# Kernel optimization log

Measured on AMD Instinct MI355X. Metric: run time of the kernel, lower is better.

The kernel has to match this reference:

```python
import jax, jax.numpy as jnp
import numpy as np

N = 30000
E = 600000
IN = 64
HID = 128
EPS = 1e-5
HEADS_PER_LAYER = (4, 4, 1)


def _bn(x, g, b):
    # eval-mode BatchNorm: running_mean=0, running_var=1
    return x * (g / np.sqrt(1.0 + EPS)) + b


def _segment_softmax(e, dst, n):
    m = jax.ops.segment_max(e, dst, num_segments=n)
    ex = jnp.exp(e - m[dst])
    s = jax.ops.segment_sum(ex, dst, num_segments=n)
    return ex / (s[dst] + 1e-16)


def _gcn_conv(x, w, b, src, dst, norm, n):
    m = (x @ w)[src] * norm[:, None]            # [E+N, HID]
    return jax.ops.segment_sum(m, dst, num_segments=n) + b


def _gat_conv(x, w, a_src, a_dst, b, src, dst, n, heads):
    C = HID // heads
    xh = (x @ w).reshape(n, heads, C)
    asrc = (xh * a_src.reshape(heads, C)).sum(-1)   # [N, heads]
    adst = (xh * a_dst.reshape(heads, C)).sum(-1)
    e = jax.nn.leaky_relu(asrc[src] + adst[dst], 0.2)  # [E+N, heads]
    alpha = _segment_softmax(e, dst, n)
    out = jax.ops.segment_sum(xh[src] * alpha[:, :, None], dst, num_segments=n)
    return out.reshape(n, HID) + b


def _forward(x, gcn_in_w, gcn_in_b, gcn_res_w, gcn_res_b, gcn_w, gcn_b,
             gcn_bn_g, gcn_bn_b, gcn_c1w, gcn_c1b, gcn_c2w, gcn_c2b,
             gcn_c3w, gcn_c3b, gat_in_w, gat_in_b, gat_w, gat_asrc,
             gat_adst, gat_b, gat_bn_g, gat_bn_b, feat_imp, gat_c1w,
             gat_c1b, gat_cbn_g, gat_cbn_b, gat_c2w, gat_c2b, gat_c3w,
             gat_c3b, fin_w, fin_b, fin_bn_g, fin_bn_b, fin2_w, fin2_b,
             edge_index):
    n = x.shape[0]
    loop = jnp.arange(n, dtype=edge_index.dtype)
    src = jnp.concatenate([edge_index[0], loop])  # add self-loops
    dst = jnp.concatenate([edge_index[1], loop])
    # GCN symmetric normalization (with self-loops)
    deg = jax.ops.segment_sum(jnp.ones_like(dst, dtype=x.dtype), dst, num_segments=n)
    dis = jnp.where(deg > 0, jax.lax.rsqrt(jnp.maximum(deg, 1.0)), 0.0)
    norm = dis[src] * dis[dst]

    # ---- GCN branch (eval: dropout = identity, self-attn skipped since N>5000) ----
    xp = x @ gcn_in_w + gcn_in_b
    res = x @ gcn_res_w + gcn_res_b
    for i in range(3):
        xn = _gcn_conv(xp, gcn_w[i], gcn_b[i], src, dst, norm, n)
        xn = jax.nn.relu(_bn(xn, gcn_bn_g[i], gcn_bn_b[i]))
        if i % 2 == 1:
            xp = xn + res
            res = xp
        else:
            xp = xn
    h = jax.nn.relu(xp @ gcn_c1w + gcn_c1b)
    h = jax.nn.relu(h @ gcn_c2w + gcn_c2b)
    gcn_out = h @ gcn_c3w + gcn_c3b

    # ---- GAT branch ----
    xg = x @ gat_in_w + gat_in_b
    for i in range(3):
        xg = _gat_conv(xg, gat_w[i], gat_asrc[i], gat_adst[i], gat_b[i],
                       src, dst, n, HEADS_PER_LAYER[i])
        xg = jax.nn.elu(_bn(xg, gat_bn_g[i], gat_bn_b[i]))
    xg = xg * feat_imp
    h = jax.nn.relu(xg @ gat_c1w + gat_c1b)
    h = _bn(h, gat_cbn_g, gat_cbn_b)
    h = jax.nn.relu(h @ gat_c2w + gat_c2b)
    gat_out = h @ gat_c3w + gat_c3b

    # ---- fusion: N > 10000 -> weighted blend path ----
    fused = 0.6 * gcn_out + 0.4 * gat_out
    h = jax.nn.relu(fused @ fin_w + fin_b)
    h = _bn(h, fin_bn_g, fin_bn_b)
    return h @ fin2_w + fin2_b  # [N, 2]


def setup_inputs() -> dict:
    key = jax.random.key(0)
    ks = iter(jax.random.split(key, 64))

    def nrm(shape, scale=1.0):
        return jax.random.normal(next(ks), shape, dtype=jnp.float32) * scale

    s_in = 1.0 / np.sqrt(IN)
    s_h = 1.0 / np.sqrt(HID)
    inp = {}
    inp['x'] = nrm((N, IN))
    inp['edge_index'] = jax.random.randint(next(ks), (2, E), 0, N, dtype=jnp.int32)
    inp['gcn_in_w'] = nrm((IN, HID), s_in); inp['gcn_in_b'] = nrm((HID,), 0.01)
    inp['gcn_res_w'] = nrm((IN, HID), s_in); inp['gcn_res_b'] = nrm((HID,), 0.01)
    inp['gcn_w'] = nrm((3, HID, HID), s_h); inp['gcn_b'] = nrm((3, HID), 0.01)
    inp['gcn_bn_g'] = 1.0 + nrm((3, HID), 0.1); inp['gcn_bn_b'] = nrm((3, HID), 0.1)
    inp['gcn_c1w'] = nrm((HID, 64), s_h); inp['gcn_c1b'] = nrm((64,), 0.01)
    inp['gcn_c2w'] = nrm((64, 32), 0.125); inp['gcn_c2b'] = nrm((32,), 0.01)
    inp['gcn_c3w'] = nrm((32, HID), 0.18); inp['gcn_c3b'] = nrm((HID,), 0.01)
    inp['gat_in_w'] = nrm((IN, HID), s_in); inp['gat_in_b'] = nrm((HID,), 0.01)
    inp['gat_w'] = nrm((3, HID, HID), s_h)
    inp['gat_asrc'] = nrm((3, HID), s_h); inp['gat_adst'] = nrm((3, HID), s_h)
    inp['gat_b'] = nrm((3, HID), 0.01)
    inp['gat_bn_g'] = 1.0 + nrm((3, HID), 0.1); inp['gat_bn_b'] = nrm((3, HID), 0.1)
    inp['feat_imp'] = 1.0 + nrm((HID,), 0.1)
    inp['gat_c1w'] = nrm((HID, 64), s_h); inp['gat_c1b'] = nrm((64,), 0.01)
    inp['gat_cbn_g'] = 1.0 + nrm((64,), 0.1); inp['gat_cbn_b'] = nrm((64,), 0.1)
    inp['gat_c2w'] = nrm((64, 32), 0.125); inp['gat_c2b'] = nrm((32,), 0.01)
    inp['gat_c3w'] = nrm((32, HID), 0.18); inp['gat_c3b'] = nrm((HID,), 0.01)
    inp['fin_w'] = nrm((HID, 64), s_h); inp['fin_b'] = nrm((64,), 0.01)
    inp['fin_bn_g'] = 1.0 + nrm((64,), 0.1); inp['fin_bn_b'] = nrm((64,), 0.1)
    inp['fin2_w'] = nrm((64, 2), 0.125); inp['fin2_b'] = nrm((2,), 0.01)
    return inp


def reference(x, edge_index, gcn_in_w, gcn_in_b, gcn_res_w, gcn_res_b, gcn_w,
              gcn_b, gcn_bn_g, gcn_bn_b, gcn_c1w, gcn_c1b, gcn_c2w, gcn_c2b,
              gcn_c3w, gcn_c3b, gat_in_w, gat_in_b, gat_w, gat_asrc, gat_adst,
              gat_b, gat_bn_g, gat_bn_b, feat_imp, gat_c1w, gat_c1b, gat_cbn_g,
              gat_cbn_b, gat_c2w, gat_c2b, gat_c3w, gat_c3b, fin_w, fin_b,
              fin_bn_g, fin_bn_b, fin2_w, fin2_b):
    return _forward(x, gcn_in_w, gcn_in_b, gcn_res_w, gcn_res_b, gcn_w, gcn_b,
                    gcn_bn_g, gcn_bn_b, gcn_c1w, gcn_c1b, gcn_c2w, gcn_c2b,
                    gcn_c3w, gcn_c3b, gat_in_w, gat_in_b, gat_w, gat_asrc,
                    gat_adst, gat_b, gat_bn_g, gat_bn_b, feat_imp, gat_c1w,
                    gat_c1b, gat_cbn_g, gat_cbn_b, gat_c2w, gat_c2b, gat_c3w,
                    gat_c3b, fin_w, fin_b, fin_bn_g, fin_bn_b, fin2_w, fin2_b,
                    edge_index)
```

## Files before the change

kernel.cpp:

```cpp
#include <hip/hip_runtime.h>
#include <hip/hip_fp16.h>

#define RSQ_BN 0.9999950000374997f

typedef _Float16 f16x8 __attribute__((ext_vector_type(8)));
typedef float f32x4 __attribute__((ext_vector_type(4)));

union H8u { uint4 u4; __half h[8]; };
union H4u { uint2 u2; __half h[4]; };

__device__ __forceinline__ float leaky02(float x) { return x > 0.f ? x : 0.2f * x; }

__device__ __forceinline__ float4 ld4(const float* p) {
    return *reinterpret_cast<const float4*>(p);
}
__device__ __forceinline__ void ld8(float* d, const float* p) {
    float4 u = ld4(p), v = ld4(p + 4);
    d[0] = u.x; d[1] = u.y; d[2] = u.z; d[3] = u.w;
    d[4] = v.x; d[5] = v.y; d[6] = v.z; d[7] = v.w;
}


__global__ void hist_k(const int* __restrict__ edst, int* __restrict__ cnt, int E, int EN) {
    int i = blockIdx.x * 256 + threadIdx.x;
    if (i >= EN) return;
    int d = (i < E) ? edst[i] : (i - E);
    atomicAdd(&cnt[d], 1);
}

__global__ __launch_bounds__(256)
void scanA_k(const int* __restrict__ cnt, int* __restrict__ rowptr,
             int* __restrict__ bsum, int n) {
    __shared__ int sh[256];
    int t = threadIdx.x;
    int i = blockIdx.x * 256 + t;
    int v = (i < n) ? cnt[i] : 0;
    sh[t] = v;
    __syncthreads();
#pragma unroll
    for (int off = 1; off < 256; off <<= 1) {
        int u = 0;
        if (t >= off) u = sh[t - off];
        __syncthreads();
        sh[t] += u;
        __syncthreads();
    }
    if (i < n) rowptr[i] = sh[t] - v;
    if (t == 255) bsum[blockIdx.x] = sh[255];
}

__global__ __launch_bounds__(256)
void scanB_k(int* __restrict__ bsum, int nb) {
    __shared__ int sh[256];
    int t = threadIdx.x;
    int v = (t < nb) ? bsum[t] : 0;
    sh[t] = v;
    __syncthreads();
#pragma unroll
    for (int off = 1; off < 256; off <<= 1) {
        int u = 0;
        if (t >= off) u = sh[t - off];
        __syncthreads();
        sh[t] += u;
        __syncthreads();
    }
    if (t < nb) bsum[t] = sh[t] - v;
}

__global__ __launch_bounds__(256)
void scanC_k(const int* __restrict__ cnt, const int* __restrict__ bsum,
             int* __restrict__ rowptr, int* __restrict__ cursor,
             float* __restrict__ dis, int n, int EN) {
    int i = blockIdx.x * 256 + threadIdx.x;
    if (i < n) {
        int r = rowptr[i] + bsum[blockIdx.x];
        rowptr[i] = r;
        cursor[i] = r;
        dis[i] = rsqrtf((float)cnt[i]);
    }
    if (i == 0) rowptr[n] = EN;
}

__global__ void scatter_k(const int* __restrict__ esrc, const int* __restrict__ edst,
                          int* __restrict__ cursor, int* __restrict__ colidx, int E, int EN) {
    int i = blockIdx.x * 256 + threadIdx.x;
    if (i >= EN) return;
    int s, d;
    if (i < E) { s = esrc[i]; d = edst[i]; }
    else       { s = i - E; d = s; }
    int pos = atomicAdd(&cursor[d], 1);
    colidx[pos] = s;
}


__global__ void wtx_all_k(const float* __restrict__ gcn_in_w, const float* __restrict__ gcn_res_w,
                          const float* __restrict__ gat_in_w,
                          const float* __restrict__ gcn_w, const float* __restrict__ gat_w,
                          const float* __restrict__ gcn_c1w, const float* __restrict__ gat_c1w,
                          const float* __restrict__ gcn_c3w, const float* __restrict__ gat_c3w,
                          const float* __restrict__ fin_w,
                          const float* __restrict__ gcn_c2w, const float* __restrict__ gat_c2w,
                          const float* __restrict__ gat_asrc, const float* __restrict__ gat_adst,
                          __half* __restrict__ WTin, __half* __restrict__ WTg,
                          __half* __restrict__ WTa, __half* __restrict__ WTc1,
                          __half* __restrict__ WTc3, __half* __restrict__ WTfin,
                          __half* __restrict__ WTc2, __half* __restrict__ WTd) {
    int idx = blockIdx.x * 256 + threadIdx.x;
    const float* src;
    __half* dst;
    int K, M, o;
    if (idx < 24576) {
        int mi = idx >> 13; o = idx & 8191;
        src = mi == 0 ? gcn_in_w : (mi == 1 ? gcn_res_w : gat_in_w);
        dst = WTin + mi * 8192; K = 64; M = 128;
    } else if (idx < 73728) {
        int r = idx - 24576; int mi = r >> 14; o = r & 16383;
        src = gcn_w + mi * 16384; dst = WTg + mi * 16384; K = 128; M = 128;
    } else if (idx < 122880) {
        int r = idx - 73728; int mi = r >> 14; o = r & 16383;
        src = gat_w + mi * 16384; dst = WTa + mi * 16384; K = 128; M = 128;
    } else if (idx < 139264) {
        int r = idx - 122880; int mi = r >> 13; o = r & 8191;
        src = mi ? gat_c1w : gcn_c1w; dst = WTc1 + mi * 8192; K = 128; M = 64;
    } else if (idx < 147456) {
        int r = idx - 139264; int mi = r >> 12; o = r & 4095;
        src = mi ? gat_c3w : gcn_c3w; dst = WTc3 + mi * 4096; K = 32; M = 128;
    } else if (idx < 155648) {
        o = idx - 147456; src = fin_w; dst = WTfin; K = 128; M = 64;
    } else if (idx < 159744) {
        int r = idx - 155648; int mi = r >> 11; o = r & 2047;
        src = mi ? gat_c2w : gcn_c2w; dst = WTc2 + mi * 2048; K = 64; M = 32;
    } else if (idx < 165888) {
        int r = idx - 159744;
        int layer = r >> 11; o = r & 2047;
        int col = o >> 7, k = o & 127;
        int hh = (layer < 2) ? 4 : 1;
        int C = 128 / hh;
        float v = 0.f;
        if (col < hh) {
            const float* w = gat_w + (size_t)(layer * 128 + k) * 128 + col * C;
            const float* av = gat_asrc + layer * 128 + col * C;
            for (int c2 = 0; c2 < C; ++c2) v += w[c2] * av[c2];
        } else if (col >= 8 && col < 8 + hh) {
            int hthis = col - 8;
            const float* w = gat_w + (size_t)(layer * 128 + k) * 128 + hthis * C;
            const float* av = gat_adst + layer * 128 + hthis * C;
            for (int c2 = 0; c2 < C; ++c2) v += w[c2] * av[c2];
        }
        WTd[(size_t)layer * 2048 + o] = (__half)v;
        return;
    } else return;
    int mcol = o / K, k = o - mcol * K;
    dst[o] = (__half)src[k * M + mcol];
}


__device__ __forceinline__ f16x8 mk_af(const float* xr, int kb) {
    float4 v0 = ld4(xr + kb), v1 = ld4(xr + kb + 4);
    f16x8 af;
    af[0] = (_Float16)v0.x; af[1] = (_Float16)v0.y;
    af[2] = (_Float16)v0.z; af[3] = (_Float16)v0.w;
    af[4] = (_Float16)v1.x; af[5] = (_Float16)v1.y;
    af[6] = (_Float16)v1.z; af[7] = (_Float16)v1.w;
    return af;
}

__global__ __launch_bounds__(256)
void mfma_lin3_k(const float* __restrict__ X, const __half* __restrict__ WTin,
                 const float* __restrict__ b0, __half* __restrict__ Y0,
                 const float* __restrict__ b1, __half* __restrict__ Y1,
                 const float* __restrict__ b2, __half* __restrict__ Y2,
                 int n, int gper) {
    constexpr int K = 64, CT = 8;
    int set = blockIdx.x / gper, blk = blockIdx.x % gper;
    const __half* WT = WTin + (size_t)set * 8192;
    const float* bi = set == 0 ? b0 : (set == 1 ? b1 : b2);
    __half* Y = set == 0 ? Y0 : (set == 1 ? Y1 : Y2);
    int wave = threadIdx.x >> 6, lane = threadIdx.x & 63;
    int m = lane & 15, quad = lane >> 4;
    int row0 = blk * 64 + wave * 16;
    int arow = min(row0 + m, n - 1);
    const float* xr = X + (size_t)arow * K;
    f32x4 acc[CT];
#pragma unroll
    for (int ct = 0; ct < CT; ++ct) acc[ct] = (f32x4){0.f, 0.f, 0.f, 0.f};
#pragma unroll
    for (int k32 = 0; k32 < K / 32; ++k32) {
        int kb = k32 * 32 + quad * 8;
        f16x8 af = mk_af(xr, kb);
#pragma unroll
        for (int ct = 0; ct < CT; ++ct) {
            f16x8 bf = *reinterpret_cast<const f16x8*>(WT + (size_t)(ct * 16 + m) * K + kb);
            acc[ct] = __builtin_amdgcn_mfma_f32_16x16x32_f16(bf, af, acc[ct], 0, 0, 0);
        }
    }
    int row = row0 + m;
    if (row < n) {
#pragma unroll
        for (int ct = 0; ct < CT; ++ct) {
            int col = ct * 16 + quad * 4;
            float4 bv = ld4(bi + col);
            H4u w;
            w.h[0] = (__half)(acc[ct][0] + bv.x);
            w.h[1] = (__half)(acc[ct][1] + bv.y);
            w.h[2] = (__half)(acc[ct][2] + bv.z);
            w.h[3] = (__half)(acc[ct][3] + bv.w);
            *reinterpret_cast<uint2*>(Y + (size_t)row * 128 + col) = w.u2;
        }
    }
}


__global__ __launch_bounds__(256)
void dual128_mfma_k(const __half* __restrict__ Xg, const __half* __restrict__ WTg,
                    __half* __restrict__ Yg,
                    const __half* __restrict__ Xa, const __half* __restrict__ WTa,
                    __half* __restrict__ Ya,
                    const float* __restrict__ dis,
                    const __half* __restrict__ WTd,
                    float* __restrict__ avp, float* __restrict__ bvp,
                    int hh, int n, int gper) {
    bool gat = blockIdx.x >= gper;
    int blk = gat ? blockIdx.x - gper : blockIdx.x;
    const __half* X = gat ? Xa : Xg;
    const __half* WT = gat ? WTa : WTg;
    __half* Y = gat ? Ya : Yg;
    int wave = threadIdx.x >> 6;
    int lane = threadIdx.x & 63;
    int m = lane & 15, quad = lane >> 4;
    int row0 = blk * 64 + wave * 16;
    int arow = min(row0 + m, n - 1);
    const __half* xr = X + (size_t)arow * 128;
    f32x4 acc[8];
#pragma unroll
    for (int ct = 0; ct < 8; ++ct) acc[ct] = (f32x4){0.f, 0.f, 0.f, 0.f};
    int row = row0 + m;
    if (!gat) {
#pragma unroll
        for (int k32 = 0; k32 < 4; ++k32) {
            int kb = k32 * 32 + quad * 8;
            f16x8 af = *reinterpret_cast<const f16x8*>(xr + kb);
#pragma unroll
            for (int ct = 0; ct < 8; ++ct) {
                f16x8 bf = *reinterpret_cast<const f16x8*>(WT + (size_t)(ct * 16 + m) * 128 + kb);
                acc[ct] = __builtin_amdgcn_mfma_f32_16x16x32_f16(bf, af, acc[ct], 0, 0, 0);
            }
        }
        if (row < n) {
            float dv = dis[row];
#pragma unroll
            for (int ct = 0; ct < 8; ++ct) {
                int col = ct * 16 + quad * 4;
                H4u w;
                w.h[0] = (__half)(acc[ct][0] * dv);
                w.h[1] = (__half)(acc[ct][1] * dv);
                w.h[2] = (__half)(acc[ct][2] * dv);
                w.h[3] = (__half)(acc[ct][3] * dv);
                *reinterpret_cast<uint2*>(Y + (size_t)row * 128 + col) = w.u2;
            }
        }
    } else {
        f32x4 accd = (f32x4){0.f, 0.f, 0.f, 0.f};
#pragma unroll
        for (int k32 = 0; k32 < 4; ++k32) {
            int kb = k32 * 32 + quad * 8;
            f16x8 af = *reinterpret_cast<const f16x8*>(xr + kb);
#pragma unroll
            for (int ct = 0; ct < 8; ++ct) {
                f16x8 bf = *reinterpret_cast<const f16x8*>(WT + (size_t)(ct * 16 + m) * 128 + kb);
                acc[ct] = __builtin_amdgcn_mfma_f32_16x16x32_f16(bf, af, acc[ct], 0, 0, 0);
            }
            f16x8 bd = *reinterpret_cast<const f16x8*>(WTd + (size_t)m * 128 + kb);
            accd = __builtin_amdgcn_mfma_f32_16x16x32_f16(bd, af, accd, 0, 0, 0);
        }
        if (row < n) {
#pragma unroll
            for (int ct = 0; ct < 8; ++ct) {
                int col = ct * 16 + quad * 4;
                H4u w;
                w.h[0] = (__half)acc[ct][0];
                w.h[1] = (__half)acc[ct][1];
                w.h[2] = (__half)acc[ct][2];
                w.h[3] = (__half)acc[ct][3];
                *reinterpret_cast<uint2*>(Y + (size_t)row * 128 + col) = w.u2;
            }
            if (quad == 0) {
#pragma unroll
                for (int reg = 0; reg < 4; ++reg)
                    if (reg < hh) avp[row * hh + reg] = accd[reg];
            } else if (quad == 2) {
#pragma unroll
                for (int reg = 0; reg < 4; ++reg)
                    if (reg < hh) bvp[row * hh + reg] = accd[reg];
            }
        }
    }
}


__global__ __launch_bounds__(256)
void fused_gather_k(const int* __restrict__ rowptr, const int* __restrict__ colidx,
                    const float* __restrict__ dis,
                    const __half* __restrict__ Tg, const float* __restrict__ gbias,
                    const float* __restrict__ gbng, const float* __restrict__ gbnb,
                    const __half* __restrict__ res, __half* __restrict__ Yg,
                    const __half* __restrict__ Ta, const float* __restrict__ avp,
                    const float* __restrict__ bvp, const float* __restrict__ abias,
                    const float* __restrict__ abng, const float* __restrict__ abnb,
                    const float* __restrict__ fimp, __half* __restrict__ Ya,
                    int n, int hh, int log2C) {
    int idx = blockIdx.x * 256 + threadIdx.x;
    int i = idx >> 4;
    if (i >= n) return;
    int c = (idx & 15) * 8;
    int h = c >> log2C;
    float ad = bvp[i * hh + h];
    int p0 = rowptr[i], p1 = rowptr[i + 1];
    float g[8], a[8];
#pragma unroll
    for (int t = 0; t < 8; ++t) { g[t] = 0.f; a[t] = 0.f; }
    float m = -3.0e38f, s = 0.f;

    int ng = (p1 - p0 + 3) >> 2;
    int p = p0;
    int sx[4]; float av[4], vm[4];
#pragma unroll
    for (int j = 0; j < 4; ++j) {
        int q = p0 + j;
        vm[j] = (q < p1) ? 1.f : 0.f;
        sx[j] = colidx[min(q, p1 - 1)];
    }
#pragma unroll
    for (int j = 0; j < 4; ++j) av[j] = avp[sx[j] * hh + h];

    for (int gi = 0; gi < ng; ++gi) {
        uint4 qg[4], qa[4];
#pragma unroll
        for (int j = 0; j < 4; ++j)
            qg[j] = *reinterpret_cast<const uint4*>(Tg + (size_t)sx[j] * 128 + c);
#pragma unroll
        for (int j = 0; j < 4; ++j)
            qa[j] = *reinterpret_cast<const uint4*>(Ta + (size_t)sx[j] * 128 + c);
        int pn = p + 4;
        int sn[4]; float avn[4], vmn[4];
#pragma unroll
        for (int j = 0; j < 4; ++j) {
            int q = pn + j;
            vmn[j] = (q < p1) ? 1.f : 0.f;
            sn[j] = colidx[min(max(q, p0), p1 - 1)];
        }
#pragma unroll
        for (int j = 0; j < 4; ++j) avn[j] = avp[sn[j] * hh + h];
        float e0 = vm[0] > 0.f ? leaky02(av[0] + ad) : -3.0e38f;
        float e1 = vm[1] > 0.f ? leaky02(av[1] + ad) : -3.0e38f;
        float e2 = vm[2] > 0.f ? leaky02(av[2] + ad) : -3.0e38f;
        float e3 = vm[3] > 0.f ? leaky02(av[3] + ad) : -3.0e38f;
        float mc = fmaxf(fmaxf(e0, e1), fmaxf(e2, e3));
        float mn = fmaxf(m, mc);
        float scale = __expf(m - mn);
        float w0 = __expf(e0 - mn), w1 = __expf(e1 - mn);
        float w2 = __expf(e2 - mn), w3 = __expf(e3 - mn);
        s = s * scale + (w0 + w1 + w2 + w3);
        m = mn;
        {
            H8u k0, k1, k2, k3;
            k0.u4 = qg[0]; k1.u4 = qg[1]; k2.u4 = qg[2]; k3.u4 = qg[3];
#pragma unroll
            for (int t = 0; t < 8; ++t) {
                float v = g[t];
                v = fmaf(__half2float(k0.h[t]), vm[0], v);
                v = fmaf(__half2float(k1.h[t]), vm[1], v);
                v = fmaf(__half2float(k2.h[t]), vm[2], v);
                v = fmaf(__half2float(k3.h[t]), vm[3], v);
                g[t] = v;
            }
        }
        {
            H8u k0, k1, k2, k3;
            k0.u4 = qa[0]; k1.u4 = qa[1]; k2.u4 = qa[2]; k3.u4 = qa[3];
#pragma unroll
            for (int t = 0; t < 8; ++t) {
                float v = a[t] * scale;
                v = fmaf(__half2float(k0.h[t]), w0, v);
                v = fmaf(__half2float(k1.h[t]), w1, v);
                v = fmaf(__half2float(k2.h[t]), w2, v);
                v = fmaf(__half2float(k3.h[t]), w3, v);
                a[t] = v;
            }
        }
        p = pn;
#pragma unroll
        for (int j = 0; j < 4; ++j) { sx[j] = sn[j]; av[j] = avn[j]; vm[j] = vmn[j]; }
    }

    {
        float di = dis[i];
        float bb[8], gg[8], nb[8];
        ld8(bb, gbias + c); ld8(gg, gbng + c); ld8(nb, gbnb + c);
        float o[8];
#pragma unroll
        for (int t = 0; t < 8; ++t) {
            float v = g[t] * di + bb[t];
            o[t] = fmaxf(v * (gg[t] * RSQ_BN) + nb[t], 0.f);
        }
        if (res) {
            H8u rr;
            rr.u4 = *reinterpret_cast<const uint4*>(res + (size_t)i * 128 + c);
#pragma unroll
            for (int t = 0; t < 8; ++t) o[t] += __half2float(rr.h[t]);
        }
        H8u w;
#pragma unroll
        for (int t = 0; t < 8; ++t) w.h[t] = (__half)o[t];
        *reinterpret_cast<uint4*>(Yg + (size_t)i * 128 + c) = w.u4;
    }
    {
        float si = 1.f / (s + 1e-16f);
        float bb[8], gg[8], nb[8];
        ld8(bb, abias + c); ld8(gg, abng + c); ld8(nb, abnb + c);
        float o[8];
#pragma unroll
        for (int t = 0; t < 8; ++t) {
            float v = a[t] * si + bb[t];
            v = v * (gg[t] * RSQ_BN) + nb[t];
            o[t] = v > 0.f ? v : expm1f(v);
        }
        if (fimp) {
            float ff[8]; ld8(ff, fimp + c);
#pragma unroll
            for (int t = 0; t < 8; ++t) o[t] *= ff[t];
        }
        H8u w;
#pragma unroll
        for (int t = 0; t < 8; ++t) w.h[t] = (__half)o[t];
        *reinterpret_cast<uint4*>(Ya + (size_t)i * 128 + c) = w.u4;
    }
}


__global__ __launch_bounds__(256)
void fused_tail_k(const __half* __restrict__ Xg, const __half* __restrict__ Xa,
                  const __half* __restrict__ WTc1,
                  const float* __restrict__ c1bg, const float* __restrict__ c1ba,
                  const float* __restrict__ cbng, const float* __restrict__ cbnb,
                  const __half* __restrict__ WTc2,
                  const float* __restrict__ c2bg, const float* __restrict__ c2ba,
                  const __half* __restrict__ WTc3,
                  const float* __restrict__ c3bg, const float* __restrict__ c3ba,
                  const __half* __restrict__ WTfin, const float* __restrict__ finb,
                  const float* __restrict__ fbng, const float* __restrict__ fbnb,
                  const float* __restrict__ w2, const float* __restrict__ b2,
                  float* __restrict__ out, int n) {
    __shared__ alignas(16) __half h1s[2][64][88];
    __shared__ alignas(16) __half h2s[2][64][56];
    __shared__ alignas(16) __half Fs[64][152];
    int wave = threadIdx.x >> 6, lane = threadIdx.x & 63;
    int m = lane & 15, quad = lane >> 4;
    int row0 = blockIdx.x * 64 + wave * 16;
    int lr0 = wave * 16;
    int arow = min(row0 + m, n - 1);

#pragma unroll
    for (int br = 0; br < 2; ++br) {
        const __half* xr = (br ? Xa : Xg) + (size_t)arow * 128;
        const __half* WT = WTc1 + br * 8192;
        f32x4 acc[4];
#pragma unroll
        for (int ct = 0; ct < 4; ++ct) acc[ct] = (f32x4){0.f, 0.f, 0.f, 0.f};
#pragma unroll
        for (int k32 = 0; k32 < 4; ++k32) {
            int kb = k32 * 32 + quad * 8;
            f16x8 af = *reinterpret_cast<const f16x8*>(xr + kb);
#pragma unroll
            for (int ct = 0; ct < 4; ++ct) {
                f16x8 bf = *reinterpret_cast<const f16x8*>(WT + (ct * 16 + m) * 128 + kb);
                acc[ct] = __builtin_amdgcn_mfma_f32_16x16x32_f16(af, bf, acc[ct], 0, 0, 0);
            }
        }
        const float* bi = br ? c1ba : c1bg;
#pragma unroll
        for (int ct = 0; ct < 4; ++ct) {
            int col = ct * 16 + m;
            float cb = bi[col];
            float cg = br ? cbng[col] * RSQ_BN : 1.f;
            float cbb = br ? cbnb[col] : 0.f;
#pragma unroll
            for (int reg = 0; reg < 4; ++reg) {
                float v = fmaxf(acc[ct][reg] + cb, 0.f) * cg + cbb;
                h1s[br][lr0 + quad * 4 + reg][col] = (__half)v;
            }
        }
    }
    __syncthreads();
#pragma unroll
    for (int br = 0; br < 2; ++br) {
        f32x4 acc[2];
        acc[0] = (f32x4){0.f, 0.f, 0.f, 0.f};
        acc[1] = (f32x4){0.f, 0.f, 0.f, 0.f};
        const __half* WT = WTc2 + br * 2048;
#pragma unroll
        for (int k32 = 0; k32 < 2; ++k32) {
            int kb = k32 * 32 + quad * 8;
            f16x8 af = *reinterpret_cast<const f16x8*>(&h1s[br][lr0 + m][kb]);
#pragma unroll
            for (int ct = 0; ct < 2; ++ct) {
                f16x8 bf = *reinterpret_cast<const f16x8*>(WT + (ct * 16 + m) * 64 + kb);
                acc[ct] = __builtin_amdgcn_mfma_f32_16x16x32_f16(af, bf, acc[ct], 0, 0, 0);
            }
        }
        const float* bi = br ? c2ba : c2bg;
#pragma unroll
        for (int ct = 0; ct < 2; ++ct) {
            int col = ct * 16 + m;
            float cb = bi[col];
#pragma unroll
            for (int reg = 0; reg < 4; ++reg) {
                float v = fmaxf(acc[ct][reg] + cb, 0.f);
                h2s[br][lr0 + quad * 4 + reg][col] = (__half)v;
            }
        }
    }
    __syncthreads();
    {
        f32x4 ag[8], aa[8];
#pragma unroll
        for (int ct = 0; ct < 8; ++ct) {
            ag[ct] = (f32x4){0.f, 0.f, 0.f, 0.f};
            aa[ct] = (f32x4){0.f, 0.f, 0.f, 0.f};
        }
        int kb = quad * 8;
        f16x8 afg = *reinterpret_cast<const f16x8*>(&h2s[0][lr0 + m][kb]);
        f16x8 afa = *reinterpret_cast<const f16x8*>(&h2s[1][lr0 + m][kb]);
#pragma unroll
        for (int ct = 0; ct < 8; ++ct) {
            f16x8 bfg = *reinterpret_cast<const f16x8*>(WTc3 + (ct * 16 + m) * 32 + kb);
            f16x8 bfa = *reinterpret_cast<const f16x8*>(WTc3 + 4096 + (ct * 16 + m) * 32 + kb);
            ag[ct] = __builtin_amdgcn_mfma_f32_16x16x32_f16(afg, bfg, ag[ct], 0, 0, 0);
            aa[ct] = __builtin_amdgcn_mfma_f32_16x16x32_f16(afa, bfa, aa[ct], 0, 0, 0);
        }
#pragma unroll
        for (int ct = 0; ct < 8; ++ct) {
            int col = ct * 16 + m;
            float cb = 0.6f * c3bg[col] + 0.4f * c3ba[col];
#pragma unroll
            for (int reg = 0; reg < 4; ++reg) {
                float v = 0.6f * ag[ct][reg] + 0.4f * aa[ct][reg] + cb;
                Fs[lr0 + quad * 4 + reg][col] = (__half)v;
            }
        }
    }
    __syncthreads();
    {
        f32x4 acc[4];
#pragma unroll
        for (int ct = 0; ct < 4; ++ct) acc[ct] = (f32x4){0.f, 0.f, 0.f, 0.f};
#pragma unroll
        for (int k32 = 0; k32 < 4; ++k32) {
            int kb = k32 * 32 + quad * 8;
            f16x8 af = *reinterpret_cast<const f16x8*>(&Fs[lr0 + m][kb]);
#pragma unroll
            for (int ct = 0; ct < 4; ++ct) {
                f16x8 bf = *reinterpret_cast<const f16x8*>(WTfin + (ct * 16 + m) * 128 + kb);
                acc[ct] = __builtin_amdgcn_mfma_f32_16x16x32_f16(af, bf, acc[ct], 0, 0, 0);
            }
        }
        float p0[4] = {0.f, 0.f, 0.f, 0.f}, p1[4] = {0.f, 0.f, 0.f, 0.f};
#pragma unroll
        for (int ct = 0; ct < 4; ++ct) {
            int col = ct * 16 + m;
            float cb = finb[col];
            float cg = fbng[col] * RSQ_BN;
            float cbb = fbnb[col];
            float w20 = w2[2 * col], w21 = w2[2 * col + 1];
#pragma unroll
            for (int reg = 0; reg < 4; ++reg) {
                float v = fmaxf(acc[ct][reg] + cb, 0.f) * cg + cbb;
                p0[reg] += v * w20;
                p1[reg] += v * w21;
            }
        }
        for (int off = 1; off < 16; off <<= 1) {
#pragma unroll
            for (int reg = 0; reg < 4; ++reg) {
                p0[reg] += __shfl_xor(p0[reg], off);
                p1[reg] += __shfl_xor(p1[reg], off);
            }
        }
        if (m == 0) {
#pragma unroll
            for (int reg = 0; reg < 4; ++reg) {
                int row = row0 + quad * 4 + reg;
                if (row < n) {
                    out[row * 2] = p0[reg] + b2[0];
                    out[row * 2 + 1] = p1[reg] + b2[1];
                }
            }
        }
    }
}


static inline int cdiv(int a, int b) { return (a + b - 1) / b; }

extern "C" void kernel_launch(void* const* d_in, const int* in_sizes, int n_in,
                              void* d_out, int out_size, void* d_ws, size_t ws_size,
                              hipStream_t stream) {
    const float* x       = (const float*)d_in[0];
    const int*   ei      = (const int*)d_in[1];
    const float* gcn_in_w = (const float*)d_in[2];
    const float* gcn_in_b = (const float*)d_in[3];
    const float* gcn_res_w = (const float*)d_in[4];
    const float* gcn_res_b = (const float*)d_in[5];
    const float* gcn_w   = (const float*)d_in[6];
    const float* gcn_b   = (const float*)d_in[7];
    const float* gcn_bn_g = (const float*)d_in[8];
    const float* gcn_bn_b = (const float*)d_in[9];
    const float* gcn_c1w = (const float*)d_in[10];
    const float* gcn_c1b = (const float*)d_in[11];
    const float* gcn_c2w = (const float*)d_in[12];
    const float* gcn_c2b = (const float*)d_in[13];
    const float* gcn_c3w = (const float*)d_in[14];
    const float* gcn_c3b = (const float*)d_in[15];
    const float* gat_in_w = (const float*)d_in[16];
    const float* gat_in_b = (const float*)d_in[17];
    const float* gat_w   = (const float*)d_in[18];
    const float* gat_asrc = (const float*)d_in[19];
    const float* gat_adst = (const float*)d_in[20];
    const float* gat_b   = (const float*)d_in[21];
    const float* gat_bn_g = (const float*)d_in[22];
    const float* gat_bn_b = (const float*)d_in[23];
    const float* feat_imp = (const float*)d_in[24];
    const float* gat_c1w = (const float*)d_in[25];
    const float* gat_c1b = (const float*)d_in[26];
    const float* gat_cbn_g = (const float*)d_in[27];
    const float* gat_cbn_b = (const float*)d_in[28];
    const float* gat_c2w = (const float*)d_in[29];
    const float* gat_c2b = (const float*)d_in[30];
    const float* gat_c3w = (const float*)d_in[31];
    const float* gat_c3b = (const float*)d_in[32];
    const float* fin_w   = (const float*)d_in[33];
    const float* fin_b   = (const float*)d_in[34];
    const float* fin_bn_g = (const float*)d_in[35];
    const float* fin_bn_b = (const float*)d_in[36];
    const float* fin2_w  = (const float*)d_in[37];
    const float* fin2_b  = (const float*)d_in[38];

    const int N = in_sizes[0] / 64;
    const int E = in_sizes[1] / 2;
    const int EN = E + N;
    const int* esrc = ei;
    const int* edst = ei + E;

    char* wp = (char*)d_ws;
    auto alloc = [&](size_t bytes) -> void* {
        void* p = (void*)wp;
        wp += (bytes + 255) & ~(size_t)255;
        return p;
    };
    int* cnt    = (int*)alloc((size_t)N * 4);
    int* rowptr = (int*)alloc((size_t)(N + 1) * 4);
    int* cursor = (int*)alloc((size_t)N * 4);
    int* bsum   = (int*)alloc((size_t)256 * 4);
    int* colidx = (int*)alloc((size_t)EN * 4);
    float* dis  = (float*)alloc((size_t)N * 4);
    __half* A   = (__half*)alloc((size_t)N * 128 * 2);
    __half* B   = (__half*)alloc((size_t)N * 128 * 2);
    __half* G   = (__half*)alloc((size_t)N * 128 * 2);
    __half* H   = (__half*)alloc((size_t)N * 128 * 2);
    __half* R   = (__half*)alloc((size_t)N * 128 * 2);
    __half* Th1 = (__half*)alloc((size_t)N * 128 * 2);
    __half* Th2 = (__half*)alloc((size_t)N * 128 * 2);
    float* avv  = (float*)alloc((size_t)N * 4 * 4);
    float* bvv  = (float*)alloc((size_t)N * 4 * 4);
    __half* WTin = (__half*)alloc((size_t)3 * 8192 * 2);
    __half* WTg  = (__half*)alloc((size_t)3 * 16384 * 2);
    __half* WTa  = (__half*)alloc((size_t)3 * 16384 * 2);
    __half* WTc1 = (__half*)alloc((size_t)2 * 8192 * 2);
    __half* WTc3 = (__half*)alloc((size_t)2 * 4096 * 2);
    __half* WTfin = (__half*)alloc((size_t)8192 * 2);
    __half* WTc2 = (__half*)alloc((size_t)2 * 2048 * 2);
    __half* WTd  = (__half*)alloc((size_t)3 * 2048 * 2);

    const int nScanB = cdiv(N, 256);
    hipMemsetAsync(cnt, 0, (size_t)N * 4, stream);
    hist_k<<<cdiv(EN, 256), 256, 0, stream>>>(edst, cnt, E, EN);
    scanA_k<<<nScanB, 256, 0, stream>>>(cnt, rowptr, bsum, N);
    scanB_k<<<1, 256, 0, stream>>>(bsum, nScanB);
    scanC_k<<<nScanB, 256, 0, stream>>>(cnt, bsum, rowptr, cursor, dis, N, EN);
    scatter_k<<<cdiv(EN, 256), 256, 0, stream>>>(esrc, edst, cursor, colidx, E, EN);
    wtx_all_k<<<648, 256, 0, stream>>>(gcn_in_w, gcn_res_w, gat_in_w, gcn_w, gat_w,
                                       gcn_c1w, gat_c1w, gcn_c3w, gat_c3w, fin_w,
                                       gcn_c2w, gat_c2w, gat_asrc, gat_adst,
                                       WTin, WTg, WTa, WTc1, WTc3, WTfin, WTc2, WTd);

    const int g64r = cdiv(N, 64);
    const int gG   = cdiv(N, 16);

    mfma_lin3_k<<<3 * g64r, 256, 0, stream>>>(x, WTin, gcn_in_b, A, gcn_res_b, R,
                                              gat_in_b, G, N, g64r);

    const int heads_arr[3] = {4, 4, 1};
    __half* gcur = A; __half* gnxt = B;
    __half* acur = G; __half* anxt = H;
    for (int i = 0; i < 3; ++i) {
        int hh = heads_arr[i];
        int log2C = (hh == 4) ? 5 : 7;
        dual128_mfma_k<<<2 * g64r, 256, 0, stream>>>(gcur, WTg + (size_t)i * 16384, Th1,
                                                     acur, WTa + (size_t)i * 16384, Th2, dis,
                                                     WTd + (size_t)i * 2048,
                                                     avv, bvv, hh, N, g64r);
        fused_gather_k<<<gG, 256, 0, stream>>>(rowptr, colidx, dis,
                                               Th1, gcn_b + i * 128, gcn_bn_g + i * 128,
                                               gcn_bn_b + i * 128, (i == 1) ? R : nullptr, gnxt,
                                               Th2, avv, bvv, gat_b + i * 128,
                                               gat_bn_g + i * 128, gat_bn_b + i * 128,
                                               (i == 2) ? feat_imp : nullptr, anxt,
                                               N, hh, log2C);
        __half* t = gcur; gcur = gnxt; gnxt = t;
        t = acur; acur = anxt; anxt = t;
    }

    fused_tail_k<<<g64r, 256, 0, stream>>>(gcur, acur,
                                           WTc1, gcn_c1b, gat_c1b, gat_cbn_g, gat_cbn_b,
                                           WTc2, gcn_c2b, gat_c2b,
                                           WTc3, gcn_c3b, gat_c3b,
                                           WTfin, fin_b, fin_bn_g, fin_bn_b,
                                           fin2_w, fin2_b, (float*)d_out, N);
}
```

Before: 472.5 us.

## Fold input projections into first conv weights and pre-swizzle MFMA weight fragments

Precomputes composed weights (in_w @ layer0 w) and composed biases for the GCN and GAT branches, plus the attention projection of the composed weights. This removes the separate input-projection kernel and the first layer's 128x128 GEMM, replacing them with one K=64 GEMM straight from x. All transposed weight buffers are also rearranged into the per-lane MFMA fragment order, so each lane reads one contiguous 16-byte chunk. The trade-off is extra fp16 rounding of the composed weights and more serial setup work in the weight-prep kernel.

```diff
diff --git a/kernel.cpp b/kernel.cpp
--- a/kernel.cpp
+++ b/kernel.cpp
@@ -93,6 +93,24 @@
 }
 
 
+__device__ __forceinline__ float pd0_elem(const float* __restrict__ gat_w,
+                                          const float* __restrict__ gat_asrc,
+                                          const float* __restrict__ gat_adst,
+                                          int t, int col) {
+    float p = 0.f;
+    if (col < 4) {
+        const float* w = gat_w + (size_t)t * 128 + col * 32;
+        const float* av = gat_asrc + col * 32;
+        for (int c2 = 0; c2 < 32; ++c2) p += w[c2] * av[c2];
+    } else if (col >= 8 && col < 12) {
+        int hh2 = col - 8;
+        const float* w = gat_w + (size_t)t * 128 + hh2 * 32;
+        const float* av = gat_adst + hh2 * 32;
+        for (int c2 = 0; c2 < 32; ++c2) p += w[c2] * av[c2];
+    }
+    return p;
+}
+
 __global__ void wtx_all_k(const float* __restrict__ gcn_in_w, const float* __restrict__ gcn_res_w,
                           const float* __restrict__ gat_in_w,
                           const float* __restrict__ gcn_w, const float* __restrict__ gat_w,
@@ -101,10 +119,14 @@
                           const float* __restrict__ fin_w,
                           const float* __restrict__ gcn_c2w, const float* __restrict__ gat_c2w,
                           const float* __restrict__ gat_asrc, const float* __restrict__ gat_adst,
+                          const float* __restrict__ gcn_in_b, const float* __restrict__ gat_in_b,
                           __half* __restrict__ WTin, __half* __restrict__ WTg,
                           __half* __restrict__ WTa, __half* __restrict__ WTc1,
                           __half* __restrict__ WTc3, __half* __restrict__ WTfin,
-                          __half* __restrict__ WTc2, __half* __restrict__ WTd) {
+                          __half* __restrict__ WTc2, __half* __restrict__ WTd,
+                          __half* __restrict__ Mg0, __half* __restrict__ Ma0,
+                          __half* __restrict__ Da, float* __restrict__ cg0,
+                          float* __restrict__ ca0, float* __restrict__ oa) {
     int idx = blockIdx.x * 256 + threadIdx.x;
     const float* src;
     __half* dst;
@@ -133,7 +155,9 @@
     } else if (idx < 165888) {
         int r = idx - 159744;
         int layer = r >> 11; o = r & 2047;
-        int col = o >> 7, k = o & 127;
+        int j = o & 7, lane = (o >> 3) & 63, k32 = o >> 9;
+        int col = lane & 15, quad = lane >> 4;
+        int k = k32 * 32 + quad * 8 + j;
         int hh = (layer < 2) ? 4 : 1;
         int C = 128 / hh;
         float v = 0.f;
@@ -149,8 +173,61 @@
         }
         WTd[(size_t)layer * 2048 + o] = (__half)v;
         return;
+    } else if (idx < 183296) {
+        int r = idx - 165888;
+        bool isA = r >= 8192;
+        o = r & 8191;
+        int j = o & 7, lane = (o >> 3) & 63, rr = o >> 9;
+        int ct = rr >> 1, k32 = rr & 1;
+        int m = lane & 15, quad = lane >> 4;
+        int k = k32 * 32 + quad * 8 + j;
+        int col = ct * 16 + m;
+        const float* inw = isA ? gat_in_w : gcn_in_w;
+        const float* lw  = isA ? gat_w : gcn_w;
+        float v = 0.f;
+        for (int t = 0; t < 128; ++t) v += inw[k * 128 + t] * lw[(size_t)t * 128 + col];
+        (isA ? Ma0 : Mg0)[o] = (__half)v;
+        return;
+    } else if (idx < 184320) {
+        o = idx - 183296;
+        int j = o & 7, lane = (o >> 3) & 63, k32 = o >> 9;
+        int col = lane & 15, quad = lane >> 4;
+        int k = k32 * 32 + quad * 8 + j;
+        float v = 0.f;
+        if (col < 4 || (col >= 8 && col < 12)) {
+            for (int t = 0; t < 128; ++t)
+                v += gat_in_w[k * 128 + t] * pd0_elem(gat_w, gat_asrc, gat_adst, t, col);
+        }
+        Da[o] = (__half)v;
+        return;
+    } else if (idx < 184448) {
+        int col = idx - 184320;
+        float v = 0.f;
+        for (int t = 0; t < 128; ++t) v += gcn_in_b[t] * gcn_w[(size_t)t * 128 + col];
+        cg0[col] = v;
+        return;
+    } else if (idx < 184576) {
+        int col = idx - 184448;
+        float v = 0.f;
+        for (int t = 0; t < 128; ++t) v += gat_in_b[t] * gat_w[(size_t)t * 128 + col];
+        ca0[col] = v;
+        return;
+    } else if (idx < 184592) {
+        int col = idx - 184576;
+        float v = 0.f;
+        if (col < 4 || (col >= 8 && col < 12)) {
+            for (int t = 0; t < 128; ++t)
+                v += gat_in_b[t] * pd0_elem(gat_w, gat_asrc, gat_adst, t, col);
+        }
+        oa[col] = v;
+        return;
     } else return;
-    int mcol = o / K, k = o - mcol * K;
+    int j = o & 7, lane = (o >> 3) & 63, r = o >> 9;
+    int KD32 = K >> 5;
+    int ct = r / KD32, k32 = r - ct * KD32;
+    int m = lane & 15, quad = lane >> 4;
+    int k = k32 * 32 + quad * 8 + j;
+    int mcol = ct * 16 + m;
     dst[o] = (__half)src[k * M + mcol];
 }
 
@@ -165,47 +242,114 @@
     return af;
 }
 
+
 __global__ __launch_bounds__(256)
-void mfma_lin3_k(const float* __restrict__ X, const __half* __restrict__ WTin,
-                 const float* __restrict__ b0, __half* __restrict__ Y0,
-                 const float* __restrict__ b1, __half* __restrict__ Y1,
-                 const float* __restrict__ b2, __half* __restrict__ Y2,
-                 int n, int gper) {
-    constexpr int K = 64, CT = 8;
-    int set = blockIdx.x / gper, blk = blockIdx.x % gper;
-    const __half* WT = WTin + (size_t)set * 8192;
-    const float* bi = set == 0 ? b0 : (set == 1 ? b1 : b2);
-    __half* Y = set == 0 ? Y0 : (set == 1 ? Y1 : Y2);
+void dual0_mfma_k(const float* __restrict__ X,
+                  const __half* __restrict__ Mg0, const __half* __restrict__ Wres,
+                  const float* __restrict__ resb,
+                  const __half* __restrict__ Ma0, const __half* __restrict__ Da,
+                  const float* __restrict__ cg0, const float* __restrict__ ca0,
+                  const float* __restrict__ oa,
+                  const float* __restrict__ dis,
+                  __half* __restrict__ Yg, __half* __restrict__ Rout,
+                  __half* __restrict__ Ya,
+                  float* __restrict__ avp, float* __restrict__ bvp,
+                  int hh, int n, int gper) {
+    bool gat = blockIdx.x >= gper;
+    int blk = gat ? blockIdx.x - gper : blockIdx.x;
     int wave = threadIdx.x >> 6, lane = threadIdx.x & 63;
     int m = lane & 15, quad = lane >> 4;
     int row0 = blk * 64 + wave * 16;
     int arow = min(row0 + m, n - 1);
-    const float* xr = X + (size_t)arow * K;
-    f32x4 acc[CT];
-#pragma unroll
-    for (int ct = 0; ct < CT; ++ct) acc[ct] = (f32x4){0.f, 0.f, 0.f, 0.f};
-#pragma unroll
-    for (int k32 = 0; k32 < K / 32; ++k32) {
-        int kb = k32 * 32 + quad * 8;
-        f16x8 af = mk_af(xr, kb);
-#pragma unroll
-        for (int ct = 0; ct < CT; ++ct) {
-            f16x8 bf = *reinterpret_cast<const f16x8*>(WT + (size_t)(ct * 16 + m) * K + kb);
-            acc[ct] = __builtin_amdgcn_mfma_f32_16x16x32_f16(bf, af, acc[ct], 0, 0, 0);
-        }
-    }
+    const float* xr = X + (size_t)arow * 64;
+    f16x8 xf0 = mk_af(xr, quad * 8);
+    f16x8 xf1 = mk_af(xr, 32 + quad * 8);
     int row = row0 + m;
-    if (row < n) {
-#pragma unroll
-        for (int ct = 0; ct < CT; ++ct) {
-            int col = ct * 16 + quad * 4;
-            float4 bv = ld4(bi + col);
-            H4u w;
-            w.h[0] = (__half)(acc[ct][0] + bv.x);
-            w.h[1] = (__half)(acc[ct][1] + bv.y);
-            w.h[2] = (__half)(acc[ct][2] + bv.z);
-            w.h[3] = (__half)(acc[ct][3] + bv.w);
-            *reinterpret_cast<uint2*>(Y + (size_t)row * 128 + col) = w.u2;
+    f32x4 acc[8];
+    if (!gat) {
+#pragma unroll
+        for (int ct = 0; ct < 8; ++ct) acc[ct] = (f32x4){0.f, 0.f, 0.f, 0.f};
+#pragma unroll
+        for (int ct = 0; ct < 8; ++ct) {
+            f16x8 b0 = *reinterpret_cast<const f16x8*>(Mg0 + ((ct * 2 + 0) << 9) + (lane << 3));
+            f16x8 b1 = *reinterpret_cast<const f16x8*>(Mg0 + ((ct * 2 + 1) << 9) + (lane << 3));
+            acc[ct] = __builtin_amdgcn_mfma_f32_16x16x32_f16(b0, xf0, acc[ct], 0, 0, 0);
+            acc[ct] = __builtin_amdgcn_mfma_f32_16x16x32_f16(b1, xf1, acc[ct], 0, 0, 0);
+        }
+        if (row < n) {
+            float dv = dis[row];
+#pragma unroll
+            for (int ct = 0; ct < 8; ++ct) {
+                int col = ct * 16 + quad * 4;
+                float4 cb = ld4(cg0 + col);
+                H4u w;
+                w.h[0] = (__half)((acc[ct][0] + cb.x) * dv);
+                w.h[1] = (__half)((acc[ct][1] + cb.y) * dv);
+                w.h[2] = (__half)((acc[ct][2] + cb.z) * dv);
+                w.h[3] = (__half)((acc[ct][3] + cb.w) * dv);
+                *reinterpret_cast<uint2*>(Yg + (size_t)row * 128 + col) = w.u2;
+            }
+        }
+#pragma unroll
+        for (int ct = 0; ct < 8; ++ct) acc[ct] = (f32x4){0.f, 0.f, 0.f, 0.f};
+#pragma unroll
+        for (int ct = 0; ct < 8; ++ct) {
+            f16x8 b0 = *reinterpret_cast<const f16x8*>(Wres + ((ct * 2 + 0) << 9) + (lane << 3));
+            f16x8 b1 = *reinterpret_cast<const f16x8*>(Wres + ((ct * 2 + 1) << 9) + (lane << 3));
+            acc[ct] = __builtin_amdgcn_mfma_f32_16x16x32_f16(b0, xf0, acc[ct], 0, 0, 0);
+            acc[ct] = __builtin_amdgcn_mfma_f32_16x16x32_f16(b1, xf1, acc[ct], 0, 0, 0);
+        }
+        if (row < n) {
+#pragma unroll
+            for (int ct = 0; ct < 8; ++ct) {
+                int col = ct * 16 + quad * 4;
+                float4 cb = ld4(resb + col);
+                H4u w;
+                w.h[0] = (__half)(acc[ct][0] + cb.x);
+                w.h[1] = (__half)(acc[ct][1] + cb.y);
+                w.h[2] = (__half)(acc[ct][2] + cb.z);
+                w.h[3] = (__half)(acc[ct][3] + cb.w);
+                *reinterpret_cast<uint2*>(Rout + (size_t)row * 128 + col) = w.u2;
+            }
+        }
+    } else {
+        f32x4 accd = (f32x4){0.f, 0.f, 0.f, 0.f};
+#pragma unroll
+        for (int ct = 0; ct < 8; ++ct) acc[ct] = (f32x4){0.f, 0.f, 0.f, 0.f};
+#pragma unroll
+        for (int ct = 0; ct < 8; ++ct) {
+            f16x8 b0 = *reinterpret_cast<const f16x8*>(Ma0 + ((ct * 2 + 0) << 9) + (lane << 3));
+            f16x8 b1 = *reinterpret_cast<const f16x8*>(Ma0 + ((ct * 2 + 1) << 9) + (lane << 3));
+            acc[ct] = __builtin_amdgcn_mfma_f32_16x16x32_f16(b0, xf0, acc[ct], 0, 0, 0);
+            acc[ct] = __builtin_amdgcn_mfma_f32_16x16x32_f16(b1, xf1, acc[ct], 0, 0, 0);
+        }
+        {
+            f16x8 d0 = *reinterpret_cast<const f16x8*>(Da + (0 << 9) + (lane << 3));
+            f16x8 d1 = *reinterpret_cast<const f16x8*>(Da + (1 << 9) + (lane << 3));
+            accd = __builtin_amdgcn_mfma_f32_16x16x32_f16(d0, xf0, accd, 0, 0, 0);
+            accd = __builtin_amdgcn_mfma_f32_16x16x32_f16(d1, xf1, accd, 0, 0, 0);
+        }
+        if (row < n) {
+#pragma unroll
+            for (int ct = 0; ct < 8; ++ct) {
+                int col = ct * 16 + quad * 4;
+                float4 cb = ld4(ca0 + col);
+                H4u w;
+                w.h[0] = (__half)(acc[ct][0] + cb.x);
+                w.h[1] = (__half)(acc[ct][1] + cb.y);
+                w.h[2] = (__half)(acc[ct][2] + cb.z);
+                w.h[3] = (__half)(acc[ct][3] + cb.w);
+                *reinterpret_cast<uint2*>(Ya + (size_t)row * 128 + col) = w.u2;
+            }
+            if (quad == 0) {
+#pragma unroll
+                for (int reg = 0; reg < 4; ++reg)
+                    if (reg < hh) avp[row * hh + reg] = accd[reg] + oa[reg];
+            } else if (quad == 2) {
+#pragma unroll
+                for (int reg = 0; reg < 4; ++reg)
+                    if (reg < hh) bvp[row * hh + reg] = accd[reg] + oa[8 + reg];
+            }
         }
     }
 }
@@ -242,7 +386,7 @@
             f16x8 af = *reinterpret_cast<const f16x8*>(xr + kb);
 #pragma unroll
             for (int ct = 0; ct < 8; ++ct) {
-                f16x8 bf = *reinterpret_cast<const f16x8*>(WT + (size_t)(ct * 16 + m) * 128 + kb);
+                f16x8 bf = *reinterpret_cast<const f16x8*>(WT + ((ct * 4 + k32) << 9) + (lane << 3));
                 acc[ct] = __builtin_amdgcn_mfma_f32_16x16x32_f16(bf, af, acc[ct], 0, 0, 0);
             }
         }
@@ -267,10 +411,10 @@
             f16x8 af = *reinterpret_cast<const f16x8*>(xr + kb);
 #pragma unroll
             for (int ct = 0; ct < 8; ++ct) {
-                f16x8 bf = *reinterpret_cast<const f16x8*>(WT + (size_t)(ct * 16 + m) * 128 + kb);
+                f16x8 bf = *reinterpret_cast<const f16x8*>(WT + ((ct * 4 + k32) << 9) + (lane << 3));
                 acc[ct] = __builtin_amdgcn_mfma_f32_16x16x32_f16(bf, af, acc[ct], 0, 0, 0);
             }
-            f16x8 bd = *reinterpret_cast<const f16x8*>(WTd + (size_t)m * 128 + kb);
+            f16x8 bd = *reinterpret_cast<const f16x8*>(WTd + (k32 << 9) + (lane << 3));
             accd = __builtin_amdgcn_mfma_f32_16x16x32_f16(bd, af, accd, 0, 0, 0);
         }
         if (row < n) {
@@ -473,7 +617,7 @@
             f16x8 af = *reinterpret_cast<const f16x8*>(xr + kb);
 #pragma unroll
             for (int ct = 0; ct < 4; ++ct) {
-                f16x8 bf = *reinterpret_cast<const f16x8*>(WT + (ct * 16 + m) * 128 + kb);
+                f16x8 bf = *reinterpret_cast<const f16x8*>(WT + ((ct * 4 + k32) << 9) + (lane << 3));
                 acc[ct] = __builtin_amdgcn_mfma_f32_16x16x32_f16(af, bf, acc[ct], 0, 0, 0);
             }
         }
@@ -504,7 +648,7 @@
             f16x8 af = *reinterpret_cast<const f16x8*>(&h1s[br][lr0 + m][kb]);
 #pragma unroll
             for (int ct = 0; ct < 2; ++ct) {
-                f16x8 bf = *reinterpret_cast<const f16x8*>(WT + (ct * 16 + m) * 64 + kb);
+                f16x8 bf = *reinterpret_cast<const f16x8*>(WT + ((ct * 2 + k32) << 9) + (lane << 3));
                 acc[ct] = __builtin_amdgcn_mfma_f32_16x16x32_f16(af, bf, acc[ct], 0, 0, 0);
             }
         }
@@ -533,8 +677,8 @@
         f16x8 afa = *reinterpret_cast<const f16x8*>(&h2s[1][lr0 + m][kb]);
 #pragma unroll
         for (int ct = 0; ct < 8; ++ct) {
-            f16x8 bfg = *reinterpret_cast<const f16x8*>(WTc3 + (ct * 16 + m) * 32 + kb);
-            f16x8 bfa = *reinterpret_cast<const f16x8*>(WTc3 + 4096 + (ct * 16 + m) * 32 + kb);
+            f16x8 bfg = *reinterpret_cast<const f16x8*>(WTc3 + (ct << 9) + (lane << 3));
+            f16x8 bfa = *reinterpret_cast<const f16x8*>(WTc3 + 4096 + (ct << 9) + (lane << 3));
             ag[ct] = __builtin_amdgcn_mfma_f32_16x16x32_f16(afg, bfg, ag[ct], 0, 0, 0);
             aa[ct] = __builtin_amdgcn_mfma_f32_16x16x32_f16(afa, bfa, aa[ct], 0, 0, 0);
         }
@@ -560,7 +704,7 @@
             f16x8 af = *reinterpret_cast<const f16x8*>(&Fs[lr0 + m][kb]);
 #pragma unroll
             for (int ct = 0; ct < 4; ++ct) {
-                f16x8 bf = *reinterpret_cast<const f16x8*>(WTfin + (ct * 16 + m) * 128 + kb);
+                f16x8 bf = *reinterpret_cast<const f16x8*>(WTfin + ((ct * 4 + k32) << 9) + (lane << 3));
                 acc[ct] = __builtin_amdgcn_mfma_f32_16x16x32_f16(af, bf, acc[ct], 0, 0, 0);
             }
         }
@@ -680,6 +824,12 @@
     __half* WTfin = (__half*)alloc((size_t)8192 * 2);
     __half* WTc2 = (__half*)alloc((size_t)2 * 2048 * 2);
     __half* WTd  = (__half*)alloc((size_t)3 * 2048 * 2);
+    __half* Mg0  = (__half*)alloc((size_t)8192 * 2);
+    __half* Ma0  = (__half*)alloc((size_t)8192 * 2);
+    __half* Da   = (__half*)alloc((size_t)1024 * 2);
+    float* cg0   = (float*)alloc((size_t)128 * 4);
+    float* ca0   = (float*)alloc((size_t)128 * 4);
+    float* oa    = (float*)alloc((size_t)16 * 4);
 
     const int nScanB = cdiv(N, 256);
     hipMemsetAsync(cnt, 0, (size_t)N * 4, stream);
@@ -688,39 +838,41 @@
     scanB_k<<<1, 256, 0, stream>>>(bsum, nScanB);
     scanC_k<<<nScanB, 256, 0, stream>>>(cnt, bsum, rowptr, cursor, dis, N, EN);
     scatter_k<<<cdiv(EN, 256), 256, 0, stream>>>(esrc, edst, cursor, colidx, E, EN);
-    wtx_all_k<<<648, 256, 0, stream>>>(gcn_in_w, gcn_res_w, gat_in_w, gcn_w, gat_w,
+    wtx_all_k<<<721, 256, 0, stream>>>(gcn_in_w, gcn_res_w, gat_in_w, gcn_w, gat_w,
                                        gcn_c1w, gat_c1w, gcn_c3w, gat_c3w, fin_w,
                                        gcn_c2w, gat_c2w, gat_asrc, gat_adst,
-                                       WTin, WTg, WTa, WTc1, WTc3, WTfin, WTc2, WTd);
+                                       gcn_in_b, gat_in_b,
+                                       WTin, WTg, WTa, WTc1, WTc3, WTfin, WTc2, WTd,
+                                       Mg0, Ma0, Da, cg0, ca0, oa);
 
     const int g64r = cdiv(N, 64);
     const int gG   = cdiv(N, 16);
 
-    mfma_lin3_k<<<3 * g64r, 256, 0, stream>>>(x, WTin, gcn_in_b, A, gcn_res_b, R,
-                                              gat_in_b, G, N, g64r);
-
-    const int heads_arr[3] = {4, 4, 1};
-    __half* gcur = A; __half* gnxt = B;
-    __half* acur = G; __half* anxt = H;
-    for (int i = 0; i < 3; ++i) {
-        int hh = heads_arr[i];
-        int log2C = (hh == 4) ? 5 : 7;
-        dual128_mfma_k<<<2 * g64r, 256, 0, stream>>>(gcur, WTg + (size_t)i * 16384, Th1,
-                                                     acur, WTa + (size_t)i * 16384, Th2, dis,
-                                                     WTd + (size_t)i * 2048,
-                                                     avv, bvv, hh, N, g64r);
-        fused_gather_k<<<gG, 256, 0, stream>>>(rowptr, colidx, dis,
-                                               Th1, gcn_b + i * 128, gcn_bn_g + i * 128,
-                                               gcn_bn_b + i * 128, (i == 1) ? R : nullptr, gnxt,
-                                               Th2, avv, bvv, gat_b + i * 128,
-                                               gat_bn_g + i * 128, gat_bn_b + i * 128,
-                                               (i == 2) ? feat_imp : nullptr, anxt,
-                                               N, hh, log2C);
-        __half* t = gcur; gcur = gnxt; gnxt = t;
-        t = acur; acur = anxt; anxt = t;
-    }
-
-    fused_tail_k<<<g64r, 256, 0, stream>>>(gcur, acur,
+    dual0_mfma_k<<<2 * g64r, 256, 0, stream>>>(x, Mg0, WTin + 8192, gcn_res_b,
+                                               Ma0, Da, cg0, ca0, oa, dis,
+                                               Th1, R, Th2, avv, bvv, 4, N, g64r);
+    fused_gather_k<<<gG, 256, 0, stream>>>(rowptr, colidx, dis,
+                                           Th1, gcn_b, gcn_bn_g, gcn_bn_b, nullptr, A,
+                                           Th2, avv, bvv, gat_b, gat_bn_g, gat_bn_b,
+                                           nullptr, G, N, 4, 5);
+    dual128_mfma_k<<<2 * g64r, 256, 0, stream>>>(A, WTg + 16384, Th1,
+                                                 G, WTa + 16384, Th2, dis,
+                                                 WTd + 2048, avv, bvv, 4, N, g64r);
+    fused_gather_k<<<gG, 256, 0, stream>>>(rowptr, colidx, dis,
+                                           Th1, gcn_b + 128, gcn_bn_g + 128, gcn_bn_b + 128,
+                                           R, B,
+                                           Th2, avv, bvv, gat_b + 128, gat_bn_g + 128,
+                                           gat_bn_b + 128, nullptr, H, N, 4, 5);
+    dual128_mfma_k<<<2 * g64r, 256, 0, stream>>>(B, WTg + 32768, Th1,
+                                                 H, WTa + 32768, Th2, dis,
+                                                 WTd + 4096, avv, bvv, 1, N, g64r);
+    fused_gather_k<<<gG, 256, 0, stream>>>(rowptr, colidx, dis,
+                                           Th1, gcn_b + 256, gcn_bn_g + 256, gcn_bn_b + 256,
+                                           nullptr, A,
+                                           Th2, avv, bvv, gat_b + 256, gat_bn_g + 256,
+                                           gat_bn_b + 256, feat_imp, G, N, 1, 7);
+
+    fused_tail_k<<<g64r, 256, 0, stream>>>(A, G,
                                            WTc1, gcn_c1b, gat_c1b, gat_cbn_g, gat_cbn_b,
                                            WTc2, gcn_c2b, gat_c2b,
                                            WTc3, gcn_c3b, gat_c3b,
```

Result: faster. 435.7 us (median of 2 runs) (-7.8%).
